# Kernel optimization log

Measured on AMD Instinct MI355X. Metric: run time of the kernel, lower is better.

## Reference

```python
import jax, jax.numpy as jnp
import numpy as np

B, N, C, K1, CO = 8, 1024, 64, 3, 64  # K1 = K+1


def _prelu(x, a):
    return jnp.where(x >= 0, x, a * x)


def setup_inputs() -> dict:
    key = jax.random.key(0)
    ks = jax.random.split(key, 12)
    X_real = jax.random.normal(ks[0], (B, N, C), jnp.float32)
    X_imag = jax.random.normal(ks[1], (B, N, C), jnp.float32)
    # complex laplacian polynomial stack (B, K+1, N, N), scaled like a normalized laplacian
    L_real = jax.random.normal(ks[2], (B, K1, N, N), jnp.float32) * 0.03
    L_imag = jax.random.normal(ks[3], (B, K1, N, N), jnp.float32) * 0.03
    # Chebyshev complex weights: uniform(-stdv, stdv) then normalized to unit magnitude
    stdv = 1.0 / np.sqrt(CO)
    wr = jax.random.uniform(ks[4], (K1, C, CO), jnp.float32, -stdv, stdv)
    wi = jax.random.uniform(ks[5], (K1, C, CO), jnp.float32, -stdv, stdv)
    mag = jnp.sqrt(wr ** 2 + wi ** 2)
    w_real, w_imag = wr / mag, wi / mag
    # CVLinear(2C, 1): complex weight split into src (X_i) and dst (X_j) halves
    astd = 1.0 / np.sqrt(2 * C)
    a_src_r = jax.random.uniform(ks[6], (C,), jnp.float32, -astd, astd)
    a_src_i = jax.random.uniform(ks[7], (C,), jnp.float32, -astd, astd)
    a_dst_r = jax.random.uniform(ks[8], (C,), jnp.float32, -astd, astd)
    a_dst_i = jax.random.uniform(ks[9], (C,), jnp.float32, -astd, astd)
    attn_b_r = jax.random.uniform(ks[10], (), jnp.float32, -astd, astd)
    attn_b_i = jax.random.uniform(ks[11], (), jnp.float32, -astd, astd)
    alpha_r = jnp.float32(0.25)  # CPReLU slopes
    alpha_i = jnp.float32(0.25)
    return dict(X_real=X_real, X_imag=X_imag, L_real=L_real, L_imag=L_imag,
                a_src_r=a_src_r, a_src_i=a_src_i, a_dst_r=a_dst_r, a_dst_i=a_dst_i,
                attn_b_r=attn_b_r, attn_b_i=attn_b_i, alpha_r=alpha_r, alpha_i=alpha_i,
                w_real=w_real, w_imag=w_imag)


def reference(X_real, X_imag, L_real, L_imag, a_src_r, a_src_i, a_dst_r, a_dst_i,
              attn_b_r, attn_b_i, alpha_r, alpha_i, w_real, w_imag):
    # --- attention: complex linear over [X_i ; X_j], decomposed GAT-style ---
    # (z @ a) for complex z, a: real = zr@ar - zi@ai ; imag = zr@ai + zi@ar
    si_r = X_real @ a_src_r - X_imag @ a_src_i  # (B, N)
    si_i = X_real @ a_src_i + X_imag @ a_src_r
    sj_r = X_real @ a_dst_r - X_imag @ a_dst_i
    sj_i = X_real @ a_dst_i + X_imag @ a_dst_r
    s_r = si_r[:, :, None] + sj_r[:, None, :] + attn_b_r  # (B, N, N) scores[b,i,j]
    s_i = si_i[:, :, None] + sj_i[:, None, :] + attn_b_i
    # CPReLU: PReLU on real and imag parts independently
    s_r = _prelu(s_r, alpha_r)
    s_i = _prelu(s_i, alpha_i)
    # PhaseSoftMax(dim=1): softmax over magnitudes along axis 1, keep phase
    mag = jnp.sqrt(s_r ** 2 + s_i ** 2)
    scale = jax.nn.softmax(mag, axis=1) / jnp.maximum(mag, 1e-12)
    a_r, a_i = scale * s_r, scale * s_i  # complex attn weights (B, N, N)
    # modulate complex laplacian: L * attn (broadcast over K dim)
    Lm_r = L_real * a_r[:, None] - L_imag * a_i[:, None]  # (B, K+1, N, N)
    Lm_i = L_real * a_i[:, None] + L_imag * a_r[:, None]
    # --- Chebyshev sum: sum_k (L_k X) W_k, complex ---
    LX_r = jnp.einsum('bknm,bmc->bknc', Lm_r, X_real) - jnp.einsum('bknm,bmc->bknc', Lm_i, X_imag)
    LX_i = jnp.einsum('bknm,bmc->bknc', Lm_r, X_imag) + jnp.einsum('bknm,bmc->bknc', Lm_i, X_real)
    out_r = jnp.einsum('bknc,kco->bno', LX_r, w_real) - jnp.einsum('bknc,kco->bno', LX_i, w_imag)
    out_i = jnp.einsum('bknc,kco->bno', LX_r, w_imag) + jnp.einsum('bknc,kco->bno', LX_i, w_real)
    return jnp.stack([out_r, out_i])  # (2, B, N, C_out)
```

## Files before the change

### kernel.cpp

```cpp
#include <hip/hip_runtime.h>

typedef __attribute__((ext_vector_type(8))) short bf16x8;
typedef __attribute__((ext_vector_type(4))) float f32x4;
typedef unsigned int uint32;
typedef unsigned short u16;

#define BN 1024

__device__ __align__(16) float g_stats[6 * 8192];
__device__ __align__(16) u16   g_Xt[8 * 16 * 2 * 64 * 64];
__device__ __align__(16) u16   g_wt[6 * 64 * 192];
__device__ __align__(16) float g_part[1024 * 6144];

__device__ __forceinline__ u16 f2bf(float x) {
    uint32 u = __float_as_uint(x);
    u += 0x7fffu + ((u >> 16) & 1u);
    return (u16)(u >> 16);
}
__device__ __forceinline__ float bf2f(u16 h) {
    return __uint_as_float(((uint32)h) << 16);
}

__global__ void k_sisj(const float* __restrict__ Xr, const float* __restrict__ Xi,
                       const float* __restrict__ asr, const float* __restrict__ asi,
                       const float* __restrict__ adr, const float* __restrict__ adi) {
    int wid = threadIdx.x >> 6, lane = threadIdx.x & 63;
    int bn = blockIdx.x * 4 + wid;
    float xr = Xr[(size_t)bn * 64 + lane], xi = Xi[(size_t)bn * 64 + lane];
    float r0 = asr[lane], i0 = asi[lane], r1 = adr[lane], i1 = adi[lane];
    float v0 = xr * r0 - xi * i0;
    float v1 = xr * i0 + xi * r0;
    float v2 = xr * r1 - xi * i1;
    float v3 = xr * i1 + xi * r1;
    #pragma unroll
    for (int off = 32; off; off >>= 1) {
        v0 += __shfl_xor(v0, off);
        v1 += __shfl_xor(v1, off);
        v2 += __shfl_xor(v2, off);
        v3 += __shfl_xor(v3, off);
    }
    if (lane == 0) {
        g_stats[bn]         = v0;
        g_stats[8192 + bn]  = v1;
        g_stats[16384 + bn] = v2;
        g_stats[24576 + bn] = v3;
    }
}

__global__ void k_mz(const float* __restrict__ pbr, const float* __restrict__ pbi,
                     const float* __restrict__ par, const float* __restrict__ pai) {
    int wid = threadIdx.x >> 6, lane = threadIdx.x & 63;
    int bj = blockIdx.x * 4 + wid;
    int b = bj >> 10;
    float br = pbr[0], bi = pbi[0], ar = par[0], ai = pai[0];
    float sjrv = g_stats[16384 + bj], sjiv = g_stats[24576 + bj];
    float mags[16];
    float mx = 0.0f;
    #pragma unroll
    for (int t = 0; t < 16; ++t) {
        int i = t * 64 + lane;
        float sr = g_stats[b * BN + i] + sjrv + br;
        float si = g_stats[8192 + b * BN + i] + sjiv + bi;
        sr = sr >= 0.f ? sr : ar * sr;
        si = si >= 0.f ? si : ai * si;
        float m = sqrtf(sr * sr + si * si);
        mags[t] = m;
        mx = fmaxf(mx, m);
    }
    #pragma unroll
    for (int off = 32; off; off >>= 1) mx = fmaxf(mx, __shfl_xor(mx, off));
    float s = 0.f;
    #pragma unroll
    for (int t = 0; t < 16; ++t) s += __expf(mags[t] - mx);
    #pragma unroll
    for (int off = 32; off; off >>= 1) s += __shfl_xor(s, off);
    if (lane == 0) { g_stats[32768 + bj] = mx; g_stats[40960 + bj] = s; }
}

__global__ void k_xt(const float* __restrict__ Xr, const float* __restrict__ Xi) {
    int b = blockIdx.x >> 4, q = blockIdx.x & 15;
    __shared__ float xs[2][64][65];
    int tid = threadIdx.x;
    #pragma unroll 4
    for (int rep = 0; rep < 32; ++rep) {
        int idx = rep * 256 + tid;
        int p = idx >> 12, j = (idx >> 6) & 63, c = idx & 63;
        const float* src = p ? Xi : Xr;
        xs[p][j][c] = src[((size_t)b * BN + q * 64 + j) * 64 + c];
    }
    __syncthreads();
    #pragma unroll
    for (int rep = 0; rep < 4; ++rep) {
        int idx = rep * 256 + tid;
        int p = idx >> 9, c = (idx >> 3) & 63, j8 = idx & 7;
        union { u16 h[8]; uint4 v; } pk;
        #pragma unroll
        for (int jj = 0; jj < 8; ++jj) pk.h[jj] = f2bf(xs[p][j8 * 8 + jj][c]);
        *(uint4*)&g_Xt[(size_t)(((b * 16 + q) * 2 + p) * 64 + c) * 64 + j8 * 8] = pk.v;
    }
}

__global__ void k_wt(const float* __restrict__ wr, const float* __restrict__ wi) {
    int t = blockIdx.x * 256 + threadIdx.x;
    int o = t & 63, kc = t >> 6;
    float vr = wr[t], vi = wi[t];
    u16 rh = f2bf(vr);
    u16 rl = f2bf(vr - bf2f(rh));
    u16 ih = f2bf(vi);
    u16 il = f2bf(vi - bf2f(ih));
    g_wt[(0 * 64 + o) * 192 + kc] = rh;
    g_wt[(1 * 64 + o) * 192 + kc] = rl;
    g_wt[(2 * 64 + o) * 192 + kc] = ih;
    g_wt[(3 * 64 + o) * 192 + kc] = il;
    g_wt[(4 * 64 + o) * 192 + kc] = (u16)(ih ^ 0x8000u);
    g_wt[(5 * 64 + o) * 192 + kc] = (u16)(il ^ 0x8000u);
}

__global__ __launch_bounds__(256) void k_main(
    const float* __restrict__ Lr, const float* __restrict__ Li,
    const float* __restrict__ pbr, const float* __restrict__ pbi,
    const float* __restrict__ par, const float* __restrict__ pai) {
    __shared__ __align__(16) u16 smem[16128];
    __shared__ __align__(16) float sA[2][16];
    u16* lmS = smem;
    u16* xS  = smem + 6912;

    int tid = threadIdx.x, wid = tid >> 6, lane = tid & 63;
    int jh = blockIdx.x & 1, it = (blockIdx.x >> 1) & 63, b = blockIdx.x >> 7;
    int i0 = it * 16;

    const float* sjr_g = g_stats + 16384;
    const float* sji_g = g_stats + 24576;
    const float* Mv_g  = g_stats + 32768;
    const float* Zv_g  = g_stats + 40960;

    if (tid < 32) {
        int p = tid >> 4, i = tid & 15;
        sA[p][i] = g_stats[p * 8192 + b * BN + i0 + i];
    }

    f32x4 zz = {0.f, 0.f, 0.f, 0.f};
    f32x4 accr[4], acci[4];
    #pragma unroll
    for (int nt = 0; nt < 4; ++nt) { accr[nt] = zz; acci[nt] = zz; }

    float brv = pbr[0], biv = pbi[0], alrv = par[0], aliv = pai[0];

    int ti = tid >> 4, tj4 = tid & 15;

    __syncthreads();
    float sirv = sA[0][ti], siiv = sA[1][ti];

    for (int qi = 0; qi < 8; ++qi) {
        int q = jh * 8 + qi;
        int j0 = q * 64;
        #pragma unroll
        for (int s = 0; s < 4; ++s) {
            int idx = s * 256 + tid;
            int p = idx >> 9, c = (idx >> 3) & 63, j8 = idx & 7;
            uint4 v = *(const uint4*)&g_Xt[(size_t)(((b * 16 + q) * 2 + p) * 64 + c) * 64 + j8 * 8];
            *(uint4*)(xS + (p * 64 + c) * 72 + j8 * 8) = v;
        }
        int jj0 = j0 + tj4 * 4;
        float4 A = *(const float4*)&sjr_g[b * BN + jj0];
        float4 Bv = *(const float4*)&sji_g[b * BN + jj0];
        float4 C = *(const float4*)&Mv_g[b * BN + jj0];
        float4 D = *(const float4*)&Zv_g[b * BN + jj0];
        float sjr4[4] = {A.x, A.y, A.z, A.w};
        float sji4[4] = {Bv.x, Bv.y, Bv.z, Bv.w};
        float M4[4]   = {C.x, C.y, C.z, C.w};
        float Z4[4]   = {D.x, D.y, D.z, D.w};
        float arj[4], aij[4];
        #pragma unroll
        for (int e = 0; e < 4; ++e) {
            float sr = sirv + sjr4[e] + brv;
            float si = siiv + sji4[e] + biv;
            sr = sr >= 0.f ? sr : alrv * sr;
            si = si >= 0.f ? si : aliv * si;
            float mg = sqrtf(sr * sr + si * si);
            float sc = __expf(mg - M4[e]) / (Z4[e] * fmaxf(mg, 1e-12f));
            arj[e] = sc * sr;
            aij[e] = sc * si;
        }
        #pragma unroll
        for (int k = 0; k < 3; ++k) {
            size_t lbase = ((size_t)(b * 3 + k) * BN + (i0 + ti)) * BN + jj0;
            float4 r4 = *(const float4*)&Lr[lbase];
            float4 s4 = *(const float4*)&Li[lbase];
            float lr4[4] = {r4.x, r4.y, r4.z, r4.w};
            float li4[4] = {s4.x, s4.y, s4.z, s4.w};
            union { u16 h[4]; uint2 v; } pr, pi;
            #pragma unroll
            for (int e = 0; e < 4; ++e) {
                float mr = lr4[e] * arj[e] - li4[e] * aij[e];
                float mi = lr4[e] * aij[e] + li4[e] * arj[e];
                pr.h[e] = f2bf(mr);
                pi.h[e] = f2bf(mi);
            }
            *(uint2*)(lmS + ((k * 2 + 0) * 16 + ti) * 72 + tj4 * 4) = pr.v;
            *(uint2*)(lmS + ((k * 2 + 1) * 16 + ti) * 72 + tj4 * 4) = pi.v;
        }
        __syncthreads();
        if (wid < 3) {
            int arow = lane & 15, kb = (lane >> 4) * 8;
            #pragma unroll
            for (int ks = 0; ks < 2; ++ks) {
                int kc = ks * 32 + kb;
                bf16x8 aR = *(const bf16x8*)(lmS + ((wid * 2 + 0) * 16 + arow) * 72 + kc);
                bf16x8 aI = *(const bf16x8*)(lmS + ((wid * 2 + 1) * 16 + arow) * 72 + kc);
                bf16x8 aIn;
                #pragma unroll
                for (int z = 0; z < 8; ++z) aIn[z] = (short)(aI[z] ^ (short)0x8000);
                #pragma unroll
                for (int nt = 0; nt < 4; ++nt) {
                    int crow = nt * 16 + arow;
                    bf16x8 xr = *(const bf16x8*)(xS + (0 * 64 + crow) * 72 + kc);
                    bf16x8 xi = *(const bf16x8*)(xS + (1 * 64 + crow) * 72 + kc);
                    accr[nt] = __builtin_amdgcn_mfma_f32_16x16x32_bf16(aR,  xr, accr[nt], 0, 0, 0);
                    accr[nt] = __builtin_amdgcn_mfma_f32_16x16x32_bf16(aIn, xi, accr[nt], 0, 0, 0);
                    acci[nt] = __builtin_amdgcn_mfma_f32_16x16x32_bf16(aR,  xi, acci[nt], 0, 0, 0);
                    acci[nt] = __builtin_amdgcn_mfma_f32_16x16x32_bf16(aI,  xr, acci[nt], 0, 0, 0);
                }
            }
        }
        __syncthreads();
    }

    if (wid < 3) {
        size_t base = (size_t)blockIdx.x * 6144;
        #pragma unroll
        for (int p = 0; p < 2; ++p) {
            #pragma unroll
            for (int nt = 0; nt < 4; ++nt) {
                f32x4 fr = p ? acci[nt] : accr[nt];
                #pragma unroll
                for (int r = 0; r < 4; ++r) {
                    int row = (lane >> 4) * 4 + r;
                    int kc = wid * 64 + nt * 16 + (lane & 15);
                    g_part[base + (size_t)(p * 16 + row) * 192 + kc] = fr[r];
                }
            }
        }
    }
}

__global__ __launch_bounds__(256) void k_out(float* __restrict__ out) {
    __shared__ __align__(16) u16 LXs[12800];
    int tid = threadIdx.x, wid = tid >> 6, lane = tid & 63;
    int b = blockIdx.x >> 6, it = blockIdx.x & 63, i0 = it * 16;
    size_t p0 = (size_t)((b * 64 + it) * 2 + 0) * 6144;
    size_t p1 = p0 + 6144;

    #pragma unroll
    for (int rep = 0; rep < 6; ++rep) {
        int idx = rep * 256 + tid;
        float4 a = *(const float4*)&g_part[p0 + (size_t)idx * 4];
        float4 c = *(const float4*)&g_part[p1 + (size_t)idx * 4];
        float s[4] = {a.x + c.x, a.y + c.y, a.z + c.z, a.w + c.w};
        int f0 = idx * 4;
        int rc = f0 / 3072, rem = f0 - rc * 3072;
        int row = rem / 192, kc = rem - row * 192;
        #pragma unroll
        for (int t = 0; t < 4; ++t) {
            float v = s[t];
            u16 hi = f2bf(v);
            u16 lo = f2bf(v - bf2f(hi));
            LXs[((rc * 2 + 0) * 16 + row) * 200 + kc + t] = hi;
            LXs[((rc * 2 + 1) * 16 + row) * 200 + kc + t] = lo;
        }
    }
    __syncthreads();

    f32x4 zz = {0.f, 0.f, 0.f, 0.f};
    f32x4 o_r = zz, o_i = zz;
    int arow = lane & 15, kb = (lane >> 4) * 8;
    int o = wid * 16 + arow;
    #pragma unroll
    for (int ks = 0; ks < 6; ++ks) {
        int kc = ks * 32 + kb;
        bf16x8 Arh = *(const bf16x8*)(LXs + (0 * 16 + arow) * 200 + kc);
        bf16x8 Arl = *(const bf16x8*)(LXs + (1 * 16 + arow) * 200 + kc);
        bf16x8 Aih = *(const bf16x8*)(LXs + (2 * 16 + arow) * 200 + kc);
        bf16x8 Ail = *(const bf16x8*)(LXs + (3 * 16 + arow) * 200 + kc);
        bf16x8 Wrh  = *(const bf16x8*)&g_wt[(0 * 64 + o) * 192 + kc];
        bf16x8 Wrl  = *(const bf16x8*)&g_wt[(1 * 64 + o) * 192 + kc];
        bf16x8 Wih  = *(const bf16x8*)&g_wt[(2 * 64 + o) * 192 + kc];
        bf16x8 Wil  = *(const bf16x8*)&g_wt[(3 * 64 + o) * 192 + kc];
        bf16x8 Wihn = *(const bf16x8*)&g_wt[(4 * 64 + o) * 192 + kc];
        bf16x8 Wiln = *(const bf16x8*)&g_wt[(5 * 64 + o) * 192 + kc];
        o_r = __builtin_amdgcn_mfma_f32_16x16x32_bf16(Arh, Wrh,  o_r, 0, 0, 0);
        o_r = __builtin_amdgcn_mfma_f32_16x16x32_bf16(Arh, Wrl,  o_r, 0, 0, 0);
        o_r = __builtin_amdgcn_mfma_f32_16x16x32_bf16(Arl, Wrh,  o_r, 0, 0, 0);
        o_r = __builtin_amdgcn_mfma_f32_16x16x32_bf16(Aih, Wihn, o_r, 0, 0, 0);
        o_r = __builtin_amdgcn_mfma_f32_16x16x32_bf16(Aih, Wiln, o_r, 0, 0, 0);
        o_r = __builtin_amdgcn_mfma_f32_16x16x32_bf16(Ail, Wihn, o_r, 0, 0, 0);
        o_i = __builtin_amdgcn_mfma_f32_16x16x32_bf16(Arh, Wih,  o_i, 0, 0, 0);
        o_i = __builtin_amdgcn_mfma_f32_16x16x32_bf16(Arh, Wil,  o_i, 0, 0, 0);
        o_i = __builtin_amdgcn_mfma_f32_16x16x32_bf16(Arl, Wih,  o_i, 0, 0, 0);
        o_i = __builtin_amdgcn_mfma_f32_16x16x32_bf16(Aih, Wrh,  o_i, 0, 0, 0);
        o_i = __builtin_amdgcn_mfma_f32_16x16x32_bf16(Aih, Wrl,  o_i, 0, 0, 0);
        o_i = __builtin_amdgcn_mfma_f32_16x16x32_bf16(Ail, Wrh,  o_i, 0, 0, 0);
    }
    #pragma unroll
    for (int r = 0; r < 4; ++r) {
        int i = (lane >> 4) * 4 + r;
        size_t off = ((size_t)b * BN + i0 + i) * 64 + o;
        out[off] = o_r[r];
        out[524288 + off] = o_i[r];
    }
}

extern "C" void kernel_launch(void* const* d_in, const int* in_sizes, int n_in,
                              void* d_out, int out_size, void* d_ws, size_t ws_size,
                              hipStream_t stream) {
    const float* Xr  = (const float*)d_in[0];
    const float* Xi  = (const float*)d_in[1];
    const float* Lr  = (const float*)d_in[2];
    const float* Li  = (const float*)d_in[3];
    const float* asr = (const float*)d_in[4];
    const float* asi = (const float*)d_in[5];
    const float* adr = (const float*)d_in[6];
    const float* adi = (const float*)d_in[7];
    const float* pbr = (const float*)d_in[8];
    const float* pbi = (const float*)d_in[9];
    const float* par = (const float*)d_in[10];
    const float* pai = (const float*)d_in[11];
    const float* wr  = (const float*)d_in[12];
    const float* wi  = (const float*)d_in[13];
    float* out = (float*)d_out;

    k_sisj<<<2048, 256, 0, stream>>>(Xr, Xi, asr, asi, adr, adi);
    k_mz<<<2048, 256, 0, stream>>>(pbr, pbi, par, pai);
    k_xt<<<128, 256, 0, stream>>>(Xr, Xi);
    k_wt<<<48, 256, 0, stream>>>(wr, wi);
    k_main<<<1024, 256, 0, stream>>>(Lr, Li, pbr, pbi, par, pai);
    k_out<<<512, 256, 0, stream>>>(out);
}
```

Before: 75.77 us.

## Split j-range four ways and register-prefetch next L and X tiles

The j dimension of the main kernel is now split into four quarters instead of halves, doubling the grid to 2048 blocks, and the partial-sum buffer and reduction in k_out grow to match. Inside the loop, the next chunk's Laplacian and X tiles are loaded into registers while the current chunk is being modulated and multiplied, so global-load latency overlaps with compute. The cost is more register pressure, twice as many partial sums to write and read back, and an extra add stage in the output kernel.

```diff
diff --git a/kernel.cpp b/kernel.cpp
--- a/kernel.cpp
+++ b/kernel.cpp
@@ -10,7 +10,7 @@
 __device__ __align__(16) float g_stats[6 * 8192];
 __device__ __align__(16) u16   g_Xt[8 * 16 * 2 * 64 * 64];
 __device__ __align__(16) u16   g_wt[6 * 64 * 192];
-__device__ __align__(16) float g_part[1024 * 6144];
+__device__ __align__(16) float g_part[2048 * 6144];
 
 __device__ __forceinline__ u16 f2bf(float x) {
     uint32 u = __float_as_uint(x);
@@ -126,7 +126,7 @@
     u16* xS  = smem + 6912;
 
     int tid = threadIdx.x, wid = tid >> 6, lane = tid & 63;
-    int jh = blockIdx.x & 1, it = (blockIdx.x >> 1) & 63, b = blockIdx.x >> 7;
+    int jh = blockIdx.x & 3, it = (blockIdx.x >> 2) & 63, b = blockIdx.x >> 8;
     int i0 = it * 16;
 
     const float* sjr_g = g_stats + 16384;
@@ -151,17 +151,39 @@
     __syncthreads();
     float sirv = sA[0][ti], siiv = sA[1][ti];
 
-    for (int qi = 0; qi < 8; ++qi) {
-        int q = jh * 8 + qi;
-        int j0 = q * 64;
+    auto loadX = [&](int q, uint4* dst) {
         #pragma unroll
         for (int s = 0; s < 4; ++s) {
             int idx = s * 256 + tid;
             int p = idx >> 9, c = (idx >> 3) & 63, j8 = idx & 7;
-            uint4 v = *(const uint4*)&g_Xt[(size_t)(((b * 16 + q) * 2 + p) * 64 + c) * 64 + j8 * 8];
-            *(uint4*)(xS + (p * 64 + c) * 72 + j8 * 8) = v;
-        }
-        int jj0 = j0 + tj4 * 4;
+            dst[s] = *(const uint4*)&g_Xt[(size_t)(((b * 16 + q) * 2 + p) * 64 + c) * 64 + j8 * 8];
+        }
+    };
+    auto loadL = [&](int q, float4* r4, float4* s4) {
+        int jj0 = q * 64 + tj4 * 4;
+        #pragma unroll
+        for (int k = 0; k < 3; ++k) {
+            size_t lbase = ((size_t)(b * 3 + k) * BN + (i0 + ti)) * BN + jj0;
+            r4[k] = *(const float4*)&Lr[lbase];
+            s4[k] = *(const float4*)&Li[lbase];
+        }
+    };
+
+    uint4 xb[4];
+    float4 lbr[3], lbi[3];
+    loadX(jh * 4, xb);
+    loadL(jh * 4, lbr, lbi);
+
+    #pragma unroll
+    for (int qi = 0; qi < 4; ++qi) {
+        int q = jh * 4 + qi;
+        int jj0 = q * 64 + tj4 * 4;
+        #pragma unroll
+        for (int s = 0; s < 4; ++s) {
+            int idx = s * 256 + tid;
+            int p = idx >> 9, c = (idx >> 3) & 63, j8 = idx & 7;
+            *(uint4*)(xS + (p * 64 + c) * 72 + j8 * 8) = xb[s];
+        }
         float4 A = *(const float4*)&sjr_g[b * BN + jj0];
         float4 Bv = *(const float4*)&sji_g[b * BN + jj0];
         float4 C = *(const float4*)&Mv_g[b * BN + jj0];
@@ -182,13 +204,16 @@
             arj[e] = sc * sr;
             aij[e] = sc * si;
         }
+        uint4 xb2[4];
+        float4 lbr2[3], lbi2[3];
+        if (qi < 3) {
+            loadX(q + 1, xb2);
+            loadL(q + 1, lbr2, lbi2);
+        }
         #pragma unroll
         for (int k = 0; k < 3; ++k) {
-            size_t lbase = ((size_t)(b * 3 + k) * BN + (i0 + ti)) * BN + jj0;
-            float4 r4 = *(const float4*)&Lr[lbase];
-            float4 s4 = *(const float4*)&Li[lbase];
-            float lr4[4] = {r4.x, r4.y, r4.z, r4.w};
-            float li4[4] = {s4.x, s4.y, s4.z, s4.w};
+            float lr4[4] = {lbr[k].x, lbr[k].y, lbr[k].z, lbr[k].w};
+            float li4[4] = {lbi[k].x, lbi[k].y, lbi[k].z, lbi[k].w};
             union { u16 h[4]; uint2 v; } pr, pi;
             #pragma unroll
             for (int e = 0; e < 4; ++e) {
@@ -224,6 +249,12 @@
             }
         }
         __syncthreads();
+        if (qi < 3) {
+            #pragma unroll
+            for (int s = 0; s < 4; ++s) xb[s] = xb2[s];
+            #pragma unroll
+            for (int k = 0; k < 3; ++k) { lbr[k] = lbr2[k]; lbi[k] = lbi2[k]; }
+        }
     }
 
     if (wid < 3) {
@@ -248,15 +279,17 @@
     __shared__ __align__(16) u16 LXs[12800];
     int tid = threadIdx.x, wid = tid >> 6, lane = tid & 63;
     int b = blockIdx.x >> 6, it = blockIdx.x & 63, i0 = it * 16;
-    size_t p0 = (size_t)((b * 64 + it) * 2 + 0) * 6144;
-    size_t p1 = p0 + 6144;
+    size_t p0 = (size_t)((b * 64 + it) * 4) * 6144;
 
     #pragma unroll
     for (int rep = 0; rep < 6; ++rep) {
         int idx = rep * 256 + tid;
-        float4 a = *(const float4*)&g_part[p0 + (size_t)idx * 4];
-        float4 c = *(const float4*)&g_part[p1 + (size_t)idx * 4];
-        float s[4] = {a.x + c.x, a.y + c.y, a.z + c.z, a.w + c.w};
+        float4 a0 = *(const float4*)&g_part[p0 + (size_t)idx * 4];
+        float4 a1 = *(const float4*)&g_part[p0 + 6144 + (size_t)idx * 4];
+        float4 a2 = *(const float4*)&g_part[p0 + 12288 + (size_t)idx * 4];
+        float4 a3 = *(const float4*)&g_part[p0 + 18432 + (size_t)idx * 4];
+        float s[4] = {a0.x + a1.x + a2.x + a3.x, a0.y + a1.y + a2.y + a3.y,
+                      a0.z + a1.z + a2.z + a3.z, a0.w + a1.w + a2.w + a3.w};
         int f0 = idx * 4;
         int rc = f0 / 3072, rem = f0 - rc * 3072;
         int row = rem / 192, kc = rem - row * 192;
@@ -333,6 +366,6 @@
     k_mz<<<2048, 256, 0, stream>>>(pbr, pbi, par, pai);
     k_xt<<<128, 256, 0, stream>>>(Xr, Xi);
     k_wt<<<48, 256, 0, stream>>>(wr, wi);
-    k_main<<<1024, 256, 0, stream>>>(Lr, Li, pbr, pbi, par, pai);
+    k_main<<<2048, 256, 0, stream>>>(Lr, Li, pbr, pbi, par, pai);
     k_out<<<512, 256, 0, stream>>>(out);
 }
```

Measured after the change: 154.7 us. 104% more time.

## Split j-range four ways, load X fragments directly, use all four waves for MFMA

Applied to the files above, without the earlier changes.

The main kernel now splits the reduction dimension into four chunks instead of two, doubling the grid to 2048 blocks. It drops the X shared-memory staging and has each wave load its B fragments straight from global memory. Work is remapped so every wave handles one 16-column slice of output channels across all three k terms, so four waves do MFMA instead of three. The output kernel now sums four partial buffers, which doubles the partial-sum traffic and its memory footprint.

```diff
diff --git a/kernel.cpp b/kernel.cpp
--- a/kernel.cpp
+++ b/kernel.cpp
@@ -10,7 +10,7 @@
 __device__ __align__(16) float g_stats[6 * 8192];
 __device__ __align__(16) u16   g_Xt[8 * 16 * 2 * 64 * 64];
 __device__ __align__(16) u16   g_wt[6 * 64 * 192];
-__device__ __align__(16) float g_part[1024 * 6144];
+__device__ __align__(16) float g_part[2048 * 6144];
 
 __device__ __forceinline__ u16 f2bf(float x) {
     uint32 u = __float_as_uint(x);
@@ -120,13 +120,11 @@
     const float* __restrict__ Lr, const float* __restrict__ Li,
     const float* __restrict__ pbr, const float* __restrict__ pbi,
     const float* __restrict__ par, const float* __restrict__ pai) {
-    __shared__ __align__(16) u16 smem[16128];
+    __shared__ __align__(16) u16 lmS[6912];
     __shared__ __align__(16) float sA[2][16];
-    u16* lmS = smem;
-    u16* xS  = smem + 6912;
 
     int tid = threadIdx.x, wid = tid >> 6, lane = tid & 63;
-    int jh = blockIdx.x & 1, it = (blockIdx.x >> 1) & 63, b = blockIdx.x >> 7;
+    int jh = blockIdx.x & 3, it = (blockIdx.x >> 2) & 63, b = blockIdx.x >> 8;
     int i0 = it * 16;
 
     const float* sjr_g = g_stats + 16384;
@@ -140,28 +138,21 @@
     }
 
     f32x4 zz = {0.f, 0.f, 0.f, 0.f};
-    f32x4 accr[4], acci[4];
-    #pragma unroll
-    for (int nt = 0; nt < 4; ++nt) { accr[nt] = zz; acci[nt] = zz; }
+    f32x4 accr[3], acci[3];
+    #pragma unroll
+    for (int k = 0; k < 3; ++k) { accr[k] = zz; acci[k] = zz; }
 
     float brv = pbr[0], biv = pbi[0], alrv = par[0], aliv = pai[0];
 
     int ti = tid >> 4, tj4 = tid & 15;
+    int arow = lane & 15, kb = (lane >> 4) * 8;
 
     __syncthreads();
     float sirv = sA[0][ti], siiv = sA[1][ti];
 
-    for (int qi = 0; qi < 8; ++qi) {
-        int q = jh * 8 + qi;
-        int j0 = q * 64;
-        #pragma unroll
-        for (int s = 0; s < 4; ++s) {
-            int idx = s * 256 + tid;
-            int p = idx >> 9, c = (idx >> 3) & 63, j8 = idx & 7;
-            uint4 v = *(const uint4*)&g_Xt[(size_t)(((b * 16 + q) * 2 + p) * 64 + c) * 64 + j8 * 8];
-            *(uint4*)(xS + (p * 64 + c) * 72 + j8 * 8) = v;
-        }
-        int jj0 = j0 + tj4 * 4;
+    for (int qi = 0; qi < 4; ++qi) {
+        int q = jh * 4 + qi;
+        int jj0 = q * 64 + tj4 * 4;
         float4 A = *(const float4*)&sjr_g[b * BN + jj0];
         float4 Bv = *(const float4*)&sji_g[b * BN + jj0];
         float4 C = *(const float4*)&Mv_g[b * BN + jj0];
@@ -200,43 +191,46 @@
             *(uint2*)(lmS + ((k * 2 + 0) * 16 + ti) * 72 + tj4 * 4) = pr.v;
             *(uint2*)(lmS + ((k * 2 + 1) * 16 + ti) * 72 + tj4 * 4) = pi.v;
         }
+        bf16x8 Bx[2][2];
+        {
+            size_t xbase = (size_t)((b * 16 + q) * 2) * 4096 + (wid * 16 + arow) * 64 + kb;
+            #pragma unroll
+            for (int p = 0; p < 2; ++p)
+                #pragma unroll
+                for (int ks = 0; ks < 2; ++ks)
+                    Bx[p][ks] = *(const bf16x8*)&g_Xt[xbase + p * 4096 + ks * 32];
+        }
         __syncthreads();
-        if (wid < 3) {
-            int arow = lane & 15, kb = (lane >> 4) * 8;
+        #pragma unroll
+        for (int k = 0; k < 3; ++k) {
             #pragma unroll
             for (int ks = 0; ks < 2; ++ks) {
                 int kc = ks * 32 + kb;
-                bf16x8 aR = *(const bf16x8*)(lmS + ((wid * 2 + 0) * 16 + arow) * 72 + kc);
-                bf16x8 aI = *(const bf16x8*)(lmS + ((wid * 2 + 1) * 16 + arow) * 72 + kc);
+                bf16x8 aR = *(const bf16x8*)(lmS + ((k * 2 + 0) * 16 + arow) * 72 + kc);
+                bf16x8 aI = *(const bf16x8*)(lmS + ((k * 2 + 1) * 16 + arow) * 72 + kc);
                 bf16x8 aIn;
                 #pragma unroll
                 for (int z = 0; z < 8; ++z) aIn[z] = (short)(aI[z] ^ (short)0x8000);
-                #pragma unroll
-                for (int nt = 0; nt < 4; ++nt) {
-                    int crow = nt * 16 + arow;
-                    bf16x8 xr = *(const bf16x8*)(xS + (0 * 64 + crow) * 72 + kc);
-                    bf16x8 xi = *(const bf16x8*)(xS + (1 * 64 + crow) * 72 + kc);
-                    accr[nt] = __builtin_amdgcn_mfma_f32_16x16x32_bf16(aR,  xr, accr[nt], 0, 0, 0);
-                    accr[nt] = __builtin_amdgcn_mfma_f32_16x16x32_bf16(aIn, xi, accr[nt], 0, 0, 0);
-                    acci[nt] = __builtin_amdgcn_mfma_f32_16x16x32_bf16(aR,  xi, acci[nt], 0, 0, 0);
-                    acci[nt] = __builtin_amdgcn_mfma_f32_16x16x32_bf16(aI,  xr, acci[nt], 0, 0, 0);
-                }
+                accr[k] = __builtin_amdgcn_mfma_f32_16x16x32_bf16(aR,  Bx[0][ks], accr[k], 0, 0, 0);
+                accr[k] = __builtin_amdgcn_mfma_f32_16x16x32_bf16(aIn, Bx[1][ks], accr[k], 0, 0, 0);
+                acci[k] = __builtin_amdgcn_mfma_f32_16x16x32_bf16(aR,  Bx[1][ks], acci[k], 0, 0, 0);
+                acci[k] = __builtin_amdgcn_mfma_f32_16x16x32_bf16(aI,  Bx[0][ks], acci[k], 0, 0, 0);
             }
         }
         __syncthreads();
     }
 
-    if (wid < 3) {
+    {
         size_t base = (size_t)blockIdx.x * 6144;
         #pragma unroll
-        for (int p = 0; p < 2; ++p) {
+        for (int k = 0; k < 3; ++k) {
             #pragma unroll
-            for (int nt = 0; nt < 4; ++nt) {
-                f32x4 fr = p ? acci[nt] : accr[nt];
+            for (int p = 0; p < 2; ++p) {
+                f32x4 fr = p ? acci[k] : accr[k];
                 #pragma unroll
                 for (int r = 0; r < 4; ++r) {
                     int row = (lane >> 4) * 4 + r;
-                    int kc = wid * 64 + nt * 16 + (lane & 15);
+                    int kc = k * 64 + wid * 16 + (lane & 15);
                     g_part[base + (size_t)(p * 16 + row) * 192 + kc] = fr[r];
                 }
             }
@@ -248,15 +242,17 @@
     __shared__ __align__(16) u16 LXs[12800];
     int tid = threadIdx.x, wid = tid >> 6, lane = tid & 63;
     int b = blockIdx.x >> 6, it = blockIdx.x & 63, i0 = it * 16;
-    size_t p0 = (size_t)((b * 64 + it) * 2 + 0) * 6144;
-    size_t p1 = p0 + 6144;
+    size_t p0 = (size_t)((b * 64 + it) * 4) * 6144;
 
     #pragma unroll
     for (int rep = 0; rep < 6; ++rep) {
         int idx = rep * 256 + tid;
-        float4 a = *(const float4*)&g_part[p0 + (size_t)idx * 4];
-        float4 c = *(const float4*)&g_part[p1 + (size_t)idx * 4];
-        float s[4] = {a.x + c.x, a.y + c.y, a.z + c.z, a.w + c.w};
+        float4 a0 = *(const float4*)&g_part[p0 + (size_t)idx * 4];
+        float4 a1 = *(const float4*)&g_part[p0 + 6144 + (size_t)idx * 4];
+        float4 a2 = *(const float4*)&g_part[p0 + 12288 + (size_t)idx * 4];
+        float4 a3 = *(const float4*)&g_part[p0 + 18432 + (size_t)idx * 4];
+        float s[4] = {a0.x + a1.x + a2.x + a3.x, a0.y + a1.y + a2.y + a3.y,
+                      a0.z + a1.z + a2.z + a3.z, a0.w + a1.w + a2.w + a3.w};
         int f0 = idx * 4;
         int rc = f0 / 3072, rem = f0 - rc * 3072;
         int row = rem / 192, kc = rem - row * 192;
@@ -333,6 +329,6 @@
     k_mz<<<2048, 256, 0, stream>>>(pbr, pbi, par, pai);
     k_xt<<<128, 256, 0, stream>>>(Xr, Xi);
     k_wt<<<48, 256, 0, stream>>>(wr, wi);
-    k_main<<<1024, 256, 0, stream>>>(Lr, Li, pbr, pbi, par, pai);
+    k_main<<<2048, 256, 0, stream>>>(Lr, Li, pbr, pbi, par, pai);
     k_out<<<512, 256, 0, stream>>>(out);
 }
```

Measured after the change: 87.33 us. 1.15x slower.
